# Performance work log

Hardware: AMD Instinct MI355X
Metric: run time of the kernel (lower is better)

## Reference

```python
import jax, jax.numpy as jnp
import numpy as np

EPS = 1e-5
N_KNN = 16


def _knn_idx(query_feat, ref_feat, k):
    # query_feat: (B, N, C), ref_feat: (B, M, C) -> idx (B, N, k) of smallest sq-dist
    q2 = jnp.sum(query_feat * query_feat, axis=-1, keepdims=True)        # (B,N,1)
    r2 = jnp.sum(ref_feat * ref_feat, axis=-1)[:, None, :]               # (B,1,M)
    d = q2 + r2 - 2.0 * jnp.einsum('bnc,bmc->bnm', query_feat, ref_feat)  # (B,N,M)
    _, idx = jax.lax.top_k(-d, k)
    return idx


def _group(x, idx):
    # x: (B, C, M), idx: (B, N, k) -> (B, C, N, k)
    B, C, M = x.shape
    _, N, k = idx.shape
    flat = jnp.broadcast_to(idx.reshape(B, 1, N * k), (B, C, N * k))
    return jnp.take_along_axis(x, flat, axis=2).reshape(B, C, N, k)


def _bn(x, g, b, m, v):
    # eval-mode BatchNorm2d over channel axis 1 of (B,C,N,k)
    inv = g / jnp.sqrt(v + EPS)
    return x * inv[None, :, None, None] + (b - m * inv)[None, :, None, None]


def setup_inputs() -> dict:
    key = jax.random.key(0)
    ks = jax.random.split(key, 24)
    B, C, N, N2 = 4, 256, 2048, 2048
    ph = 64  # pos_hidden_dim
    ah = 256  # dim * attn_hidden_multiplier = 64*4
    s = lambda fan: 1.0 / np.sqrt(fan)
    inp = {
        'pcd': jax.random.normal(ks[0], (B, 3, N), jnp.float32),
        'feat': jax.random.normal(ks[1], (B, C, N), jnp.float32),
        'pcd_feadb': jax.random.normal(ks[2], (B, 3, N2), jnp.float32),
        'feat_feadb': jax.random.normal(ks[3], (B, C, N2), jnp.float32),
        'pos_w1': jax.random.normal(ks[4], (ph, 3), jnp.float32) * s(3),
        'pos_b1': jax.random.normal(ks[5], (ph,), jnp.float32) * 0.01,
        'pos_g': jax.random.uniform(ks[6], (ph,), jnp.float32, 0.5, 1.5),
        'pos_be': jax.random.normal(ks[7], (ph,), jnp.float32) * 0.01,
        'pos_m': jax.random.normal(ks[8], (ph,), jnp.float32) * 0.1,
        'pos_v': jax.random.uniform(ks[9], (ph,), jnp.float32, 0.5, 1.5),
        'pos_w2': jax.random.normal(ks[10], (C, ph), jnp.float32) * s(ph),
        'pos_b2': jax.random.normal(ks[11], (C,), jnp.float32) * 0.01,
        'attn_w1': jax.random.normal(ks[12], (ah, C), jnp.float32) * s(C),
        'attn_b1': jax.random.normal(ks[13], (ah,), jnp.float32) * 0.01,
        'attn_g': jax.random.uniform(ks[14], (ah,), jnp.float32, 0.5, 1.5),
        'attn_be': jax.random.normal(ks[15], (ah,), jnp.float32) * 0.01,
        'attn_m': jax.random.normal(ks[16], (ah,), jnp.float32) * 0.1,
        'attn_v': jax.random.uniform(ks[17], (ah,), jnp.float32, 0.5, 1.5),
        'attn_w2': jax.random.normal(ks[18], (C, ah), jnp.float32) * s(ah),
        'attn_b2': jax.random.normal(ks[19], (C,), jnp.float32) * 0.01,
    }
    return inp


def reference(pcd, feat, pcd_feadb, feat_feadb,
              pos_w1, pos_b1, pos_g, pos_be, pos_m, pos_v, pos_w2, pos_b2,
              attn_w1, attn_b1, attn_g, attn_be, attn_m, attn_v, attn_w2, attn_b2):
    fusion_pcd = jnp.concatenate([pcd, pcd_feadb], axis=2)    # (B,3,M)
    fusion_feat = jnp.concatenate([feat, feat_feadb], axis=2)  # (B,C,M)
    # KNN in feature space: neighbors of each key point among fusion set
    idx = _knn_idx(jnp.swapaxes(feat, 1, 2), jnp.swapaxes(fusion_feat, 1, 2), N_KNN)  # (B,N,k)
    group_point = _group(fusion_pcd, idx)   # (B,3,N,k)
    group_feat = _group(fusion_feat, idx)   # (B,C,N,k)
    qk_rel = feat[:, :, :, None] - group_feat
    pos_rel = pcd[:, :, :, None] - group_point
    # pos_mlp: conv1x1 -> BN -> relu -> conv1x1
    h = jnp.einsum('oc,bcnk->bonk', pos_w1, pos_rel) + pos_b1[None, :, None, None]
    h = jax.nn.relu(_bn(h, pos_g, pos_be, pos_m, pos_v))
    pos_embedding = jnp.einsum('oc,bcnk->bonk', pos_w2, h) + pos_b2[None, :, None, None]
    # attn_mlp
    a = jnp.einsum('oc,bcnk->bonk', attn_w1, qk_rel + pos_embedding) + attn_b1[None, :, None, None]
    a = jax.nn.relu(_bn(a, attn_g, attn_be, attn_m, attn_v))
    a = jnp.einsum('oc,bcnk->bonk', attn_w2, a) + attn_b2[None, :, None, None]
    sample_weight = jax.nn.softmax(a, axis=-1)  # softmax over the k neighbors
    refined_feat = jnp.sum(sample_weight * (group_feat + pos_embedding), axis=-1)  # (B,C,N)
    return refined_feat
```

## Files before the change

kernel.cpp:

```cpp
#include <hip/hip_runtime.h>
#include <float.h>

#define CDIM 256
#define NPTS 2048
#define MPTS 4096
#define NB   4
#define KNN  16
#define COLS 64
#define NCHUNK 8
#define CSIZE  512
#define NSTEPS 16
#define QPB   256

typedef _Float16 half8 __attribute__((ext_vector_type(8)));
typedef _Float16 half4 __attribute__((ext_vector_type(4)));
typedef float    f32x4 __attribute__((ext_vector_type(4)));

__device__ __forceinline__ int swzS(int row, int byte) {
    return row * 512 + (byte ^ ((row & 7) << 4));
}
__device__ __forceinline__ int swz128(int row, int byte) {
    return row * 128 + (byte ^ ((row & 7) << 4));
}

__device__ __forceinline__ float sum16(float v) {
    v += __uint_as_float(__builtin_amdgcn_update_dpp(0, __float_as_uint(v), 0x128, 0xF, 0xF, true));
    v += __uint_as_float(__builtin_amdgcn_update_dpp(0, __float_as_uint(v), 0x124, 0xF, 0xF, true));
    v += __uint_as_float(__builtin_amdgcn_update_dpp(0, __float_as_uint(v), 0x122, 0xF, 0xF, true));
    v += __uint_as_float(__builtin_amdgcn_update_dpp(0, __float_as_uint(v), 0x121, 0xF, 0xF, true));
    return v;
}

#define CEA(x, y)                                                               \
    { unsigned lo_ = kk[x] < kk[y] ? kk[x] : kk[y];                             \
      unsigned hi_ = kk[x] < kk[y] ? kk[y] : kk[x];                             \
      kk[x] = lo_; kk[y] = hi_; }
#define CED(x, y)                                                               \
    { unsigned hi_ = td[x] > td[y] ? td[x] : td[y];                             \
      unsigned lo_ = td[x] > td[y] ? td[y] : td[x];                             \
      td[x] = hi_; td[y] = lo_; }
#define RESORT16                                                                \
    CED(0,8) CED(1,9) CED(2,10) CED(3,11) CED(4,12) CED(5,13) CED(6,14) CED(7,15) \
    CED(0,4) CED(1,5) CED(2,6) CED(3,7) CED(8,12) CED(9,13) CED(10,14) CED(11,15) \
    CED(0,2) CED(1,3) CED(4,6) CED(5,7) CED(8,10) CED(9,11) CED(12,14) CED(13,15) \
    CED(0,1) CED(2,3) CED(4,5) CED(6,7) CED(8,9) CED(10,11) CED(12,13) CED(14,15)

__global__ __launch_bounds__(256) void tposeHL2(const float* __restrict__ feat,
                                                const float* __restrict__ featdb,
                                                _Float16* __restrict__ featH,
                                                _Float16* __restrict__ featL,
                                                float* __restrict__ r2) {
    __shared__ float red[8][33];
    const int b = blockIdx.y;
    const int mt = blockIdx.x;
    const int m = threadIdx.x & 31;
    const int cp = threadIdx.x >> 5;
    const int mg = mt * 32 + m;
    const float* src = (mg < NPTS) ? (feat + (size_t)b * CDIM * NPTS + mg)
                                   : (featdb + (size_t)b * CDIM * NPTS + (mg - NPTS));
    const int c0 = cp * 32;
    float acc = 0.f;
    half8 hh[4], ll[4];
#pragma unroll
    for (int i = 0; i < 32; i++) {
        float v = src[(size_t)(c0 + i) * NPTS];
        acc += v * v;
        _Float16 h = (_Float16)v;
        hh[i >> 3][i & 7] = h;
        ll[i >> 3][i & 7] = (_Float16)(v - (float)h);
    }
    _Float16* dh = featH + ((size_t)b * MPTS + mg) * CDIM + c0;
    _Float16* dl = featL + ((size_t)b * MPTS + mg) * CDIM + c0;
#pragma unroll
    for (int i = 0; i < 4; i++) {
        *(half8*)(dh + i * 8) = hh[i];
        *(half8*)(dl + i * 8) = ll[i];
    }
    red[cp][m] = acc;
    __syncthreads();
    if (threadIdx.x < 32) {
        float s = 0.f;
#pragma unroll
        for (int j = 0; j < 8; j++) s += red[j][threadIdx.x];
        r2[b * MPTS + mt * 32 + threadIdx.x] = s;
    }
}

__global__ __launch_bounds__(256) void wcvt(const float* __restrict__ aw1,
                                            const float* __restrict__ aw2,
                                            const float* __restrict__ pw2,
                                            _Float16* __restrict__ aw1h,
                                            _Float16* __restrict__ aw2h,
                                            _Float16* __restrict__ pw2h) {
    int i = blockIdx.x * 256 + threadIdx.x;
    if (i < 65536) { aw1h[i] = (_Float16)aw1[i]; aw2h[i] = (_Float16)aw2[i]; }
    if (i < 16384) { pw2h[i] = (_Float16)pw2[i]; }
}

__global__ __launch_bounds__(1024, 2) void score_knn(const _Float16* __restrict__ featH,
                                                     const _Float16* __restrict__ featL,
                                                     const float* __restrict__ r2g,
                                                     unsigned* __restrict__ partial) {
    __shared__ __align__(16) char sbuf[65536];
    __shared__ float sr2[CSIZE];

    const int tid = threadIdx.x;
    const int lane = tid & 63, wave = tid >> 6;
    const int l15 = lane & 15, l4 = lane >> 4;
    const int chunk = blockIdx.x, qt = blockIdx.y, b = blockIdx.z;
    const int nq = qt * QPB + wave * 16 + l15;
    const int m0 = chunk * CSIZE;

    if (tid < CSIZE) sr2[tid] = r2g[b * MPTS + m0 + tid];

    half8 qh[8], ql[8];
    {
        const _Float16* qb = featH + ((size_t)b * MPTS + nq) * CDIM + l4 * 8;
        const _Float16* qL = featL + ((size_t)b * MPTS + nq) * CDIM + l4 * 8;
#pragma unroll
        for (int ks = 0; ks < 8; ks++) {
            qh[ks] = *(const half8*)(qb + ks * 32);
            ql[ks] = *(const half8*)(qL + ks * 32);
        }
    }

    int adr[8];
#pragma unroll
    for (int ks = 0; ks < 8; ks++)
        adr[ks] = (ks * 4 + l4) * 512 + ((l15 * 16) ^ ((ks & 7) << 4));

    const int srow = tid >> 5;
    const int oo = tid & 31;
    const int wadr = oo * 512 + ((srow * 16) ^ (((oo >> 2) & 7) << 4));
    const char* gH = (const char*)(featH + ((size_t)b * MPTS + m0 + srow) * CDIM) + oo * 16;
    const char* gL = (const char*)(featL + ((size_t)b * MPTS + m0 + srow) * CDIM) + oo * 16;

    unsigned td[16];
#pragma unroll
    for (int i = 0; i < 16; i++) td[i] = 0xFFFFFFFFu;

    half8 pH = *(const half8*)gH;
    half8 pL = *(const half8*)gL;
    gH += 32 * CDIM * 2;
    gL += 32 * CDIM * 2;

    for (int s = 0; s < NSTEPS; ++s) {
        char* buf = sbuf + (s & 1) * 32768;
        *(half8*)(buf + wadr)         = pH;
        *(half8*)(buf + 16384 + wadr) = pL;
        __syncthreads();

        if (s < NSTEPS - 1) {
            pH = *(const half8*)gH;
            pL = *(const half8*)gL;
            gH += 32 * CDIM * 2;
            gL += 32 * CDIM * 2;
        }

        unsigned kk[8];
#pragma unroll
        for (int sub = 0; sub < 2; ++sub) {
            f32x4 a0 = {0.f, 0.f, 0.f, 0.f};
            f32x4 a1 = {0.f, 0.f, 0.f, 0.f};
            f32x4 a2 = {0.f, 0.f, 0.f, 0.f};
#pragma unroll
            for (int ks = 0; ks < 8; ks++) {
                half8 ah = *(const half8*)(buf + adr[ks] + sub * 256);
                half8 al = *(const half8*)(buf + 16384 + adr[ks] + sub * 256);
                a0 = __builtin_amdgcn_mfma_f32_16x16x32_f16(ah, qh[ks], a0, 0, 0, 0);
                a1 = __builtin_amdgcn_mfma_f32_16x16x32_f16(ah, ql[ks], a1, 0, 0, 0);
                a2 = __builtin_amdgcn_mfma_f32_16x16x32_f16(al, qh[ks], a2, 0, 0, 0);
            }
            float4 s4 = *(const float4*)(sr2 + s * 32 + sub * 16 + 4 * l4);
            const float sv[4] = {s4.x, s4.y, s4.z, s4.w};
            const int mloc0 = s * 32 + sub * 16 + 4 * l4;
#pragma unroll
            for (int r = 0; r < 4; r++) {
                float d = fmaxf(sv[r] - 2.f * (a0[r] + a1[r] + a2[r]), 0.f);
                unsigned dq = (unsigned)(d * 4096.f);
                dq = dq > 0x7FFFF0u ? 0x7FFFF0u : dq;
                kk[sub * 4 + r] = (dq << 9) | (unsigned)(mloc0 + r);
            }
        }
        CEA(0,1) CEA(2,3) CEA(4,5) CEA(6,7)
        CEA(0,2) CEA(1,3) CEA(4,6) CEA(5,7)
        CEA(1,2) CEA(5,6) CEA(0,4) CEA(3,7)
        CEA(1,5) CEA(2,6)
        CEA(1,4) CEA(3,6)
        CEA(2,4) CEA(3,5)
        CEA(3,4)
#pragma unroll
        for (int i = 0; i < 8; i++) td[i] = td[i] < kk[i] ? td[i] : kk[i];
        RESORT16
    }

#pragma unroll
    for (int rr = 0; rr < 2; rr++) {
        const int dx = 16 << rr;
        unsigned ot[16];
#pragma unroll
        for (int e = 0; e < 16; e++) ot[e] = __shfl_xor(td[e], dx);
#pragma unroll
        for (int e = 0; e < 16; e++) {
            unsigned o = ot[15 - e];
            td[e] = td[e] < o ? td[e] : o;
        }
        RESORT16
    }
    if (l4 == 0) {
        const size_t qrow = (size_t)b * NPTS + qt * QPB + wave * 16 + l15;
#pragma unroll
        for (int e = 0; e < 16; e++)
            partial[(size_t)(chunk * 16 + e) * (NB * NPTS) + qrow] = td[e];
    }
}

__global__ __launch_bounds__(256) void merge16(const unsigned* __restrict__ partial,
                                               int* __restrict__ idxout) {
    const int row = blockIdx.x * 256 + threadIdx.x;
    unsigned long long td[16];
#pragma unroll
    for (int i = 0; i < 16; i++) td[i] = 0x8000000000ull + (unsigned long long)i;
    unsigned long long curmax = 0x800000000Full;
    for (int e = 0; e < NCHUNK * 16; e++) {
        unsigned k = partial[(size_t)e * (NB * NPTS) + row];
        unsigned long long k64 =
            (((unsigned long long)(k >> 9)) << 12) |
            (unsigned long long)((unsigned)((e >> 4) << 9) | (k & 0x1FFu));
        if (k64 < curmax) {
#pragma unroll
            for (int i_ = 0; i_ < 16; i_++) td[i_] = (td[i_] == curmax) ? k64 : td[i_];
            unsigned long long nm_ = td[0];
#pragma unroll
            for (int i_ = 1; i_ < 16; i_++) nm_ = td[i_] > nm_ ? td[i_] : nm_;
            curmax = nm_;
        }
    }
#pragma unroll
    for (int e = 0; e < 16; e++) idxout[row * 16 + e] = (int)(td[e] & 0xFFFull);
}

__global__ __launch_bounds__(512, 4) void fused_mlp6(
    const float* __restrict__ pcd, const float* __restrict__ pcddb,
    const _Float16* __restrict__ featH, const int* __restrict__ knn,
    const float* __restrict__ pw1, const float* __restrict__ pb1,
    const float* __restrict__ pg, const float* __restrict__ pbe,
    const float* __restrict__ pm, const float* __restrict__ pv,
    const _Float16* __restrict__ pw2h, const float* __restrict__ pb2,
    const _Float16* __restrict__ aw1h, const float* __restrict__ ab1,
    const float* __restrict__ ag, const float* __restrict__ abe,
    const float* __restrict__ am, const float* __restrict__ av,
    const _Float16* __restrict__ aw2h,
    float* __restrict__ out) {
    __shared__ __align__(16) _Float16 xbuf[COLS * 256];
    __shared__ __align__(16) _Float16 hbuf[COLS * 64];
    __shared__ __align__(16) float pr[3][COLS];
    __shared__ int sidx[COLS];
    __shared__ __align__(16) float ainv[256], ash2[256], pinv[64], psh[64];

    const int tid = threadIdx.x;
    const int lane = tid & 63, wave = tid >> 6;
    const int l15 = lane & 15, l4 = lane >> 4;
    const int blk = blockIdx.x;
    const int b = blk >> 9;
    const int n0 = (blk & 511) * 4;
    const int R0 = wave * 32;

    if (tid < COLS) {
        sidx[tid] = knn[(size_t)(b * NPTS + n0 + (tid >> 4)) * KNN + (tid & 15)];
    } else if (tid < COLS + 256) {
        int c = tid - COLS;
        float inv = ag[c] / sqrtf(av[c] + 1e-5f);
        ainv[c] = inv;
        ash2[c] = abe[c] - am[c] * inv + ab1[c] * inv;
    } else if (tid < COLS + 256 + 64) {
        int o = tid - COLS - 256;
        float inv = pg[o] / sqrtf(pv[o] + 1e-5f);
        pinv[o] = inv;
        psh[o] = pbe[o] - pm[o] * inv;
    }
    half8 wp[2][2];
#pragma unroll
    for (int rt = 0; rt < 2; rt++)
#pragma unroll
        for (int ks = 0; ks < 2; ks++)
            wp[rt][ks] = *(const half8*)(pw2h + (size_t)(R0 + rt * 16 + l15) * 64 +
                                         ks * 32 + l4 * 8);
    __syncthreads();

    if (tid < 3 * COLS) {
        int c = tid >> 6, col = tid & 63;
        int m = sidx[col];
        const float* pc = pcd + ((size_t)b * 3 + c) * NPTS;
        const float* px = pcddb + ((size_t)b * 3 + c) * NPTS;
        float gp = (m < NPTS) ? pc[m] : px[m - NPTS];
        pr[c][col] = pc[n0 + (col >> 4)] - gp;
    }
    const int colx = tid & 63;
    const int c0x = (tid >> 6) * 32;
    half8 fmv[4], fnv[4];
    {
        const _Float16* fmp = featH + ((size_t)b * MPTS + sidx[colx]) * CDIM + c0x;
        const _Float16* fnp = featH + ((size_t)b * MPTS + n0 + (colx >> 4)) * CDIM + c0x;
#pragma unroll
        for (int j = 0; j < 4; j++) {
            fmv[j] = *(const half8*)(fmp + j * 8);
            fnv[j] = *(const half8*)(fnp + j * 8);
        }
    }
    __syncthreads();

    {
        int col = tid >> 3, o0 = (tid & 7) * 8;
        float x0 = pr[0][col], x1 = pr[1][col], x2 = pr[2][col];
        half8 hv;
#pragma unroll
        for (int i = 0; i < 8; i++) {
            int o = o0 + i;
            float v = pw1[o * 3] * x0 + pw1[o * 3 + 1] * x1 + pw1[o * 3 + 2] * x2 + pb1[o];
            v = fmaxf(v * pinv[o] + psh[o], 0.f);
            hv[i] = (_Float16)v;
        }
        *(half8*)((char*)hbuf + swz128(col, o0 * 2)) = hv;
    }
    __syncthreads();

    f32x4 acc[2][4];
#pragma unroll
    for (int rt = 0; rt < 2; rt++)
#pragma unroll
        for (int ct = 0; ct < 4; ct++) acc[rt][ct] = (f32x4){0.f, 0.f, 0.f, 0.f};
#pragma unroll
    for (int ks = 0; ks < 2; ks++) {
        int k0 = ks * 32 + l4 * 8;
#pragma unroll
        for (int ct = 0; ct < 4; ct++) {
            half8 bb = *(const half8*)((char*)hbuf + swz128(ct * 16 + l15, k0 * 2));
            acc[0][ct] = __builtin_amdgcn_mfma_f32_16x16x32_f16(wp[0][ks], bb, acc[0][ct], 0, 0, 0);
            acc[1][ct] = __builtin_amdgcn_mfma_f32_16x16x32_f16(wp[1][ks], bb, acc[1][ct], 0, 0, 0);
        }
    }
    half4 pe4[2][4];
#pragma unroll
    for (int rt = 0; rt < 2; rt++) {
        int cb = R0 + rt * 16 + 4 * l4;
        float4 pb = *(const float4*)(pb2 + cb);
        float pbv[4] = {pb.x, pb.y, pb.z, pb.w};
#pragma unroll
        for (int ct = 0; ct < 4; ct++) {
            int col = ct * 16 + l15;
            half4 p4;
#pragma unroll
            for (int r = 0; r < 4; r++) p4[r] = (_Float16)(acc[rt][ct][r] + pbv[r]);
            pe4[rt][ct] = p4;
            *(half4*)((char*)xbuf + swzS(col, cb * 2)) = p4;
        }
    }
    __syncthreads();

#pragma unroll
    for (int j = 0; j < 4; j++) {
        int c = c0x + j * 8;
        half8 vp = *(const half8*)((char*)xbuf + swzS(colx, c * 2));
        half8 xv = fnv[j] - fmv[j] + vp;
        *(half8*)((char*)xbuf + swzS(colx, c * 2)) = xv;
    }
    half8 wa[8];
#pragma unroll
    for (int ks = 0; ks < 8; ks++)
        wa[ks] = *(const half8*)(aw1h + (size_t)(R0 + l15) * 256 + ks * 32 + l4 * 8);
    __syncthreads();

#pragma unroll
    for (int rt = 0; rt < 2; rt++)
#pragma unroll
        for (int ct = 0; ct < 4; ct++) acc[rt][ct] = (f32x4){0.f, 0.f, 0.f, 0.f};
#pragma unroll
    for (int ks = 0; ks < 8; ks++) {
        int k0 = ks * 32 + l4 * 8;
#pragma unroll
        for (int ct = 0; ct < 4; ct++) {
            half8 bb = *(const half8*)((char*)xbuf + swzS(ct * 16 + l15, k0 * 2));
            acc[0][ct] = __builtin_amdgcn_mfma_f32_16x16x32_f16(wa[ks], bb, acc[0][ct], 0, 0, 0);
        }
    }
#pragma unroll
    for (int ks = 0; ks < 8; ks++)
        wa[ks] = *(const half8*)(aw1h + (size_t)(R0 + 16 + l15) * 256 + ks * 32 + l4 * 8);
#pragma unroll
    for (int ks = 0; ks < 8; ks++) {
        int k0 = ks * 32 + l4 * 8;
#pragma unroll
        for (int ct = 0; ct < 4; ct++) {
            half8 bb = *(const half8*)((char*)xbuf + swzS(ct * 16 + l15, k0 * 2));
            acc[1][ct] = __builtin_amdgcn_mfma_f32_16x16x32_f16(wa[ks], bb, acc[1][ct], 0, 0, 0);
        }
    }
    __syncthreads();

#pragma unroll
    for (int rt = 0; rt < 2; rt++) {
        int cb = R0 + rt * 16 + 4 * l4;
        float4 iv = *(const float4*)(&ainv[cb]);
        float4 sh = *(const float4*)(&ash2[cb]);
        float ivv[4] = {iv.x, iv.y, iv.z, iv.w};
        float shv[4] = {sh.x, sh.y, sh.z, sh.w};
#pragma unroll
        for (int ct = 0; ct < 4; ct++) {
            int col = ct * 16 + l15;
            half4 h4;
#pragma unroll
            for (int r = 0; r < 4; r++)
                h4[r] = (_Float16)fmaxf(acc[rt][ct][r] * ivv[r] + shv[r], 0.f);
            *(half4*)((char*)xbuf + swzS(col, cb * 2)) = h4;
        }
    }
#pragma unroll
    for (int ks = 0; ks < 8; ks++)
        wa[ks] = *(const half8*)(aw2h + (size_t)(R0 + l15) * 256 + ks * 32 + l4 * 8);
    __syncthreads();

#pragma unroll
    for (int rt = 0; rt < 2; rt++)
#pragma unroll
        for (int ct = 0; ct < 4; ct++) acc[rt][ct] = (f32x4){0.f, 0.f, 0.f, 0.f};
#pragma unroll
    for (int ks = 0; ks < 8; ks++) {
        int k0 = ks * 32 + l4 * 8;
#pragma unroll
        for (int ct = 0; ct < 4; ct++) {
            half8 bb = *(const half8*)((char*)xbuf + swzS(ct * 16 + l15, k0 * 2));
            acc[0][ct] = __builtin_amdgcn_mfma_f32_16x16x32_f16(wa[ks], bb, acc[0][ct], 0, 0, 0);
        }
    }
#pragma unroll
    for (int ks = 0; ks < 8; ks++)
        wa[ks] = *(const half8*)(aw2h + (size_t)(R0 + 16 + l15) * 256 + ks * 32 + l4 * 8);
#pragma unroll
    for (int ks = 0; ks < 8; ks++) {
        int k0 = ks * 32 + l4 * 8;
#pragma unroll
        for (int ct = 0; ct < 4; ct++) {
            half8 bb = *(const half8*)((char*)xbuf + swzS(ct * 16 + l15, k0 * 2));
            acc[1][ct] = __builtin_amdgcn_mfma_f32_16x16x32_f16(wa[ks], bb, acc[1][ct], 0, 0, 0);
        }
    }

#pragma unroll
    for (int rt = 0; rt < 2; rt++) {
        int cb = R0 + rt * 16 + 4 * l4;
        half4 gfa[4];
#pragma unroll
        for (int ct = 0; ct < 4; ct++)
            gfa[ct] = *(const half4*)(featH +
                ((size_t)b * MPTS + sidx[ct * 16 + l15]) * CDIM + cb);
#pragma unroll
        for (int ct = 0; ct < 4; ct++) {
            float oo[4], ss[4];
#pragma unroll
            for (int r = 0; r < 4; r++) {
                float v = acc[rt][ct][r];
                v = fminf(fmaxf(v, -60.f), 60.f);
                float e = __expf(v);
                float sv = (float)gfa[ct][r] + (float)pe4[rt][ct][r];
                ss[r] = sum16(e);
                oo[r] = sum16(e * sv);
            }
            if (l15 < 4) {
                float o = l15 == 0 ? oo[0] : l15 == 1 ? oo[1] : l15 == 2 ? oo[2] : oo[3];
                float s = l15 == 0 ? ss[0] : l15 == 1 ? ss[1] : l15 == 2 ? ss[2] : ss[3];
                out[((size_t)b * CDIM + cb + l15) * NPTS + n0 + ct] =
                    o * __builtin_amdgcn_rcpf(s);
            }
        }
    }
}

extern "C" void kernel_launch(void* const* d_in, const int* in_sizes, int n_in,
                              void* d_out, int out_size, void* d_ws, size_t ws_size,
                              hipStream_t stream) {
    const float* pcd    = (const float*)d_in[0];
    const float* feat   = (const float*)d_in[1];
    const float* pcddb  = (const float*)d_in[2];
    const float* featdb = (const float*)d_in[3];
    const float* pw1 = (const float*)d_in[4];
    const float* pb1 = (const float*)d_in[5];
    const float* pg  = (const float*)d_in[6];
    const float* pbe = (const float*)d_in[7];
    const float* pm  = (const float*)d_in[8];
    const float* pv  = (const float*)d_in[9];
    const float* pw2 = (const float*)d_in[10];
    const float* pb2 = (const float*)d_in[11];
    const float* aw1 = (const float*)d_in[12];
    const float* ab1 = (const float*)d_in[13];
    const float* ag  = (const float*)d_in[14];
    const float* abe = (const float*)d_in[15];
    const float* am  = (const float*)d_in[16];
    const float* av  = (const float*)d_in[17];
    const float* aw2 = (const float*)d_in[18];
    float* out = (float*)d_out;

    char* ws = (char*)d_ws;
    _Float16* featH   = (_Float16*)(ws);
    _Float16* featL   = (_Float16*)(ws + 8388608);
    float*    ws_r2   = (float*)(ws + 16777216);
    unsigned* partial = (unsigned*)(ws + 16842752);
    int*      ws_idx  = (int*)(ws + 21037056);
    _Float16* aw1h    = (_Float16*)(ws + 21561344);
    _Float16* aw2h    = (_Float16*)(ws + 21692416);
    _Float16* pw2h    = (_Float16*)(ws + 21823488);

    wcvt<<<256, 256, 0, stream>>>(aw1, aw2, pw2, aw1h, aw2h, pw2h);
    tposeHL2<<<dim3(MPTS / 32, NB), 256, 0, stream>>>(feat, featdb, featH, featL, ws_r2);
    score_knn<<<dim3(NCHUNK, NPTS / QPB, NB), 1024, 0, stream>>>(featH, featL, ws_r2, partial);
    merge16<<<NB * NPTS / 256, 256, 0, stream>>>(partial, ws_idx);
    fused_mlp6<<<NB * (NPTS / 4), 512, 0, stream>>>(
        pcd, pcddb, featH, ws_idx,
        pw1, pb1, pg, pbe, pm, pv, pw2h, pb2,
        aw1h, ab1, ag, abe, am, av, aw2h, out);
}
```

Before: 266.9 us.

## Widen fused MLP block to eight points per block with per-wave single row tile

The fused MLP kernel now handles 8 query points (128 neighbor columns) per 1024-thread block instead of 4 points per 512-thread block. Each wave owns one 16-row output tile across 8 column tiles rather than two row tiles across 4 column tiles. This halves the global weight-fragment loads per column and removes the second reload pass of attention weights. In exchange, shared memory per block roughly doubles and the block is larger, which can lower the number of resident blocks per CU and reduce latency hiding.

```diff
diff --git a/kernel.cpp b/kernel.cpp
--- a/kernel.cpp
+++ b/kernel.cpp
@@ -6,7 +6,8 @@
 #define MPTS 4096
 #define NB   4
 #define KNN  16
-#define COLS 64
+#define COLS 128
+#define NPB  8
 #define NCHUNK 8
 #define CSIZE  512
 #define NSTEPS 16
@@ -240,7 +241,7 @@
     for (int e = 0; e < 16; e++) idxout[row * 16 + e] = (int)(td[e] & 0xFFFull);
 }
 
-__global__ __launch_bounds__(512, 4) void fused_mlp6(
+__global__ __launch_bounds__(1024, 4) void fused_mlp8(
     const float* __restrict__ pcd, const float* __restrict__ pcddb,
     const _Float16* __restrict__ featH, const int* __restrict__ knn,
     const float* __restrict__ pw1, const float* __restrict__ pb1,
@@ -262,9 +263,9 @@
     const int lane = tid & 63, wave = tid >> 6;
     const int l15 = lane & 15, l4 = lane >> 4;
     const int blk = blockIdx.x;
-    const int b = blk >> 9;
-    const int n0 = (blk & 511) * 4;
-    const int R0 = wave * 32;
+    const int b = blk >> 8;
+    const int n0 = (blk & 255) * NPB;
+    const int R0 = wave * 16;
 
     if (tid < COLS) {
         sidx[tid] = knn[(size_t)(b * NPTS + n0 + (tid >> 4)) * KNN + (tid & 15)];
@@ -279,25 +280,22 @@
         pinv[o] = inv;
         psh[o] = pbe[o] - pm[o] * inv;
     }
-    half8 wp[2][2];
-#pragma unroll
-    for (int rt = 0; rt < 2; rt++)
-#pragma unroll
-        for (int ks = 0; ks < 2; ks++)
-            wp[rt][ks] = *(const half8*)(pw2h + (size_t)(R0 + rt * 16 + l15) * 64 +
-                                         ks * 32 + l4 * 8);
+    half8 wp[2];
+#pragma unroll
+    for (int ks = 0; ks < 2; ks++)
+        wp[ks] = *(const half8*)(pw2h + (size_t)(R0 + l15) * 64 + ks * 32 + l4 * 8);
     __syncthreads();
 
     if (tid < 3 * COLS) {
-        int c = tid >> 6, col = tid & 63;
+        int c = tid >> 7, col = tid & (COLS - 1);
         int m = sidx[col];
         const float* pc = pcd + ((size_t)b * 3 + c) * NPTS;
         const float* px = pcddb + ((size_t)b * 3 + c) * NPTS;
         float gp = (m < NPTS) ? pc[m] : px[m - NPTS];
         pr[c][col] = pc[n0 + (col >> 4)] - gp;
     }
-    const int colx = tid & 63;
-    const int c0x = (tid >> 6) * 32;
+    const int colx = tid & (COLS - 1);
+    const int c0x = (tid >> 7) * 32;
     half8 fmv[4], fnv[4];
     {
         const _Float16* fmp = featH + ((size_t)b * MPTS + sidx[colx]) * CDIM + c0x;
@@ -325,34 +323,30 @@
     }
     __syncthreads();
 
-    f32x4 acc[2][4];
-#pragma unroll
-    for (int rt = 0; rt < 2; rt++)
-#pragma unroll
-        for (int ct = 0; ct < 4; ct++) acc[rt][ct] = (f32x4){0.f, 0.f, 0.f, 0.f};
+    f32x4 acc[8];
+#pragma unroll
+    for (int ct = 0; ct < 8; ct++) acc[ct] = (f32x4){0.f, 0.f, 0.f, 0.f};
 #pragma unroll
     for (int ks = 0; ks < 2; ks++) {
-        int k0 = ks * 32 + l4 * 8;
-#pragma unroll
-        for (int ct = 0; ct < 4; ct++) {
-            half8 bb = *(const half8*)((char*)hbuf + swz128(ct * 16 + l15, k0 * 2));
-            acc[0][ct] = __builtin_amdgcn_mfma_f32_16x16x32_f16(wp[0][ks], bb, acc[0][ct], 0, 0, 0);
-            acc[1][ct] = __builtin_amdgcn_mfma_f32_16x16x32_f16(wp[1][ks], bb, acc[1][ct], 0, 0, 0);
-        }
-    }
-    half4 pe4[2][4];
-#pragma unroll
-    for (int rt = 0; rt < 2; rt++) {
-        int cb = R0 + rt * 16 + 4 * l4;
+#pragma unroll
+        for (int ct = 0; ct < 8; ct++) {
+            half8 bb = *(const half8*)((char*)hbuf +
+                                       swz128(ct * 16 + l15, (ks * 32 + l4 * 8) * 2));
+            acc[ct] = __builtin_amdgcn_mfma_f32_16x16x32_f16(wp[ks], bb, acc[ct], 0, 0, 0);
+        }
+    }
+    const int cb = R0 + 4 * l4;
+    half4 pe4[8];
+    {
         float4 pb = *(const float4*)(pb2 + cb);
         float pbv[4] = {pb.x, pb.y, pb.z, pb.w};
 #pragma unroll
-        for (int ct = 0; ct < 4; ct++) {
+        for (int ct = 0; ct < 8; ct++) {
             int col = ct * 16 + l15;
             half4 p4;
 #pragma unroll
-            for (int r = 0; r < 4; r++) p4[r] = (_Float16)(acc[rt][ct][r] + pbv[r]);
-            pe4[rt][ct] = p4;
+            for (int r = 0; r < 4; r++) p4[r] = (_Float16)(acc[ct][r] + pbv[r]);
+            pe4[ct] = p4;
             *(half4*)((char*)xbuf + swzS(col, cb * 2)) = p4;
         }
     }
@@ -372,46 +366,30 @@
     __syncthreads();
 
 #pragma unroll
-    for (int rt = 0; rt < 2; rt++)
-#pragma unroll
-        for (int ct = 0; ct < 4; ct++) acc[rt][ct] = (f32x4){0.f, 0.f, 0.f, 0.f};
+    for (int ct = 0; ct < 8; ct++) acc[ct] = (f32x4){0.f, 0.f, 0.f, 0.f};
 #pragma unroll
     for (int ks = 0; ks < 8; ks++) {
         int k0 = ks * 32 + l4 * 8;
 #pragma unroll
-        for (int ct = 0; ct < 4; ct++) {
+        for (int ct = 0; ct < 8; ct++) {
             half8 bb = *(const half8*)((char*)xbuf + swzS(ct * 16 + l15, k0 * 2));
-            acc[0][ct] = __builtin_amdgcn_mfma_f32_16x16x32_f16(wa[ks], bb, acc[0][ct], 0, 0, 0);
-        }
-    }
-#pragma unroll
-    for (int ks = 0; ks < 8; ks++)
-        wa[ks] = *(const half8*)(aw1h + (size_t)(R0 + 16 + l15) * 256 + ks * 32 + l4 * 8);
-#pragma unroll
-    for (int ks = 0; ks < 8; ks++) {
-        int k0 = ks * 32 + l4 * 8;
-#pragma unroll
-        for (int ct = 0; ct < 4; ct++) {
-            half8 bb = *(const half8*)((char*)xbuf + swzS(ct * 16 + l15, k0 * 2));
-            acc[1][ct] = __builtin_amdgcn_mfma_f32_16x16x32_f16(wa[ks], bb, acc[1][ct], 0, 0, 0);
-        }
-    }
-    __syncthreads();
-
-#pragma unroll
-    for (int rt = 0; rt < 2; rt++) {
-        int cb = R0 + rt * 16 + 4 * l4;
+            acc[ct] = __builtin_amdgcn_mfma_f32_16x16x32_f16(wa[ks], bb, acc[ct], 0, 0, 0);
+        }
+    }
+    __syncthreads();
+
+    {
         float4 iv = *(const float4*)(&ainv[cb]);
         float4 sh = *(const float4*)(&ash2[cb]);
         float ivv[4] = {iv.x, iv.y, iv.z, iv.w};
         float shv[4] = {sh.x, sh.y, sh.z, sh.w};
 #pragma unroll
-        for (int ct = 0; ct < 4; ct++) {
+        for (int ct = 0; ct < 8; ct++) {
             int col = ct * 16 + l15;
             half4 h4;
 #pragma unroll
             for (int r = 0; r < 4; r++)
-                h4[r] = (_Float16)fmaxf(acc[rt][ct][r] * ivv[r] + shv[r], 0.f);
+                h4[r] = (_Float16)fmaxf(acc[ct][r] * ivv[r] + shv[r], 0.f);
             *(half4*)((char*)xbuf + swzS(col, cb * 2)) = h4;
         }
     }
@@ -421,57 +399,36 @@
     __syncthreads();
 
 #pragma unroll
-    for (int rt = 0; rt < 2; rt++)
-#pragma unroll
-        for (int ct = 0; ct < 4; ct++) acc[rt][ct] = (f32x4){0.f, 0.f, 0.f, 0.f};
+    for (int ct = 0; ct < 8; ct++) acc[ct] = (f32x4){0.f, 0.f, 0.f, 0.f};
 #pragma unroll
     for (int ks = 0; ks < 8; ks++) {
         int k0 = ks * 32 + l4 * 8;
 #pragma unroll
-        for (int ct = 0; ct < 4; ct++) {
+        for (int ct = 0; ct < 8; ct++) {
             half8 bb = *(const half8*)((char*)xbuf + swzS(ct * 16 + l15, k0 * 2));
-            acc[0][ct] = __builtin_amdgcn_mfma_f32_16x16x32_f16(wa[ks], bb, acc[0][ct], 0, 0, 0);
-        }
-    }
-#pragma unroll
-    for (int ks = 0; ks < 8; ks++)
-        wa[ks] = *(const half8*)(aw2h + (size_t)(R0 + 16 + l15) * 256 + ks * 32 + l4 * 8);
-#pragma unroll
-    for (int ks = 0; ks < 8; ks++) {
-        int k0 = ks * 32 + l4 * 8;
-#pragma unroll
-        for (int ct = 0; ct < 4; ct++) {
-            half8 bb = *(const half8*)((char*)xbuf + swzS(ct * 16 + l15, k0 * 2));
-            acc[1][ct] = __builtin_amdgcn_mfma_f32_16x16x32_f16(wa[ks], bb, acc[1][ct], 0, 0, 0);
-        }
-    }
-
-#pragma unroll
-    for (int rt = 0; rt < 2; rt++) {
-        int cb = R0 + rt * 16 + 4 * l4;
-        half4 gfa[4];
-#pragma unroll
-        for (int ct = 0; ct < 4; ct++)
-            gfa[ct] = *(const half4*)(featH +
-                ((size_t)b * MPTS + sidx[ct * 16 + l15]) * CDIM + cb);
-#pragma unroll
-        for (int ct = 0; ct < 4; ct++) {
-            float oo[4], ss[4];
-#pragma unroll
-            for (int r = 0; r < 4; r++) {
-                float v = acc[rt][ct][r];
-                v = fminf(fmaxf(v, -60.f), 60.f);
-                float e = __expf(v);
-                float sv = (float)gfa[ct][r] + (float)pe4[rt][ct][r];
-                ss[r] = sum16(e);
-                oo[r] = sum16(e * sv);
-            }
-            if (l15 < 4) {
-                float o = l15 == 0 ? oo[0] : l15 == 1 ? oo[1] : l15 == 2 ? oo[2] : oo[3];
-                float s = l15 == 0 ? ss[0] : l15 == 1 ? ss[1] : l15 == 2 ? ss[2] : ss[3];
-                out[((size_t)b * CDIM + cb + l15) * NPTS + n0 + ct] =
-                    o * __builtin_amdgcn_rcpf(s);
-            }
+            acc[ct] = __builtin_amdgcn_mfma_f32_16x16x32_f16(wa[ks], bb, acc[ct], 0, 0, 0);
+        }
+    }
+
+#pragma unroll
+    for (int ct = 0; ct < 8; ct++) {
+        half4 gfa = *(const half4*)(featH +
+            ((size_t)b * MPTS + sidx[ct * 16 + l15]) * CDIM + cb);
+        float oo[4], ss[4];
+#pragma unroll
+        for (int r = 0; r < 4; r++) {
+            float v = acc[ct][r];
+            v = fminf(fmaxf(v, -60.f), 60.f);
+            float e = __expf(v);
+            float sv = (float)gfa[r] + (float)pe4[ct][r];
+            ss[r] = sum16(e);
+            oo[r] = sum16(e * sv);
+        }
+        if (l15 < 4) {
+            float o = l15 == 0 ? oo[0] : l15 == 1 ? oo[1] : l15 == 2 ? oo[2] : oo[3];
+            float s = l15 == 0 ? ss[0] : l15 == 1 ? ss[1] : l15 == 2 ? ss[2] : ss[3];
+            out[((size_t)b * CDIM + cb + l15) * NPTS + n0 + ct] =
+                o * __builtin_amdgcn_rcpf(s);
         }
     }
 }
@@ -514,7 +471,7 @@
     tposeHL2<<<dim3(MPTS / 32, NB), 256, 0, stream>>>(feat, featdb, featH, featL, ws_r2);
     score_knn<<<dim3(NCHUNK, NPTS / QPB, NB), 1024, 0, stream>>>(featH, featL, ws_r2, partial);
     merge16<<<NB * NPTS / 256, 256, 0, stream>>>(partial, ws_idx);
-    fused_mlp6<<<NB * (NPTS / 4), 512, 0, stream>>>(
+    fused_mlp8<<<NB * (NPTS / NPB), 1024, 0, stream>>>(
         pcd, pcddb, featH, ws_idx,
         pw1, pb1, pg, pbe, pm, pv, pw2h, pb2,
         aw1h, ab1, ag, abe, am, av, aw2h, out);
```

Measured after the change: 254.4 us (median of 2 runs). -4.7%, faster.
